# Optimization experiments

Hardware: AMD Instinct MI355X
Metric: run time of the kernel (lower is better)

## Reference

```python
import jax, jax.numpy as jnp
import numpy as np

B, T, C, H = 8, 2048, 1024, 64


def build_rope_cache(seq_len, dim):
    half = dim // 2
    inv_freq = 1.0 / (10000.0 ** (jnp.arange(half, dtype=jnp.float32) / half))
    t = jnp.arange(seq_len, dtype=jnp.float32)
    freqs = t[:, None] * inv_freq[None, :]          # (T, half)
    cos = jnp.repeat(jnp.cos(freqs), 2, axis=-1)    # (T, dim) interleaved
    sin = jnp.repeat(jnp.sin(freqs), 2, axis=-1)
    return cos, sin


def apply_rope(x, cos, sin):
    # x: (B, T, H); cos/sin: (T, H)
    x1 = x[..., ::2]
    x2 = x[..., 1::2]
    rot = jnp.stack([-x2, x1], axis=-1).reshape(x.shape)
    return x * cos[None] + rot * sin[None]


def setup_inputs() -> dict:
    key = jax.random.key(0)
    kx, kq, kk, kv = jax.random.split(key, 4)
    scale = 1.0 / np.sqrt(C)
    return {
        "x": jax.random.normal(kx, (B, T, C), dtype=jnp.float32),
        "Wq": jax.random.normal(kq, (C, H), dtype=jnp.float32) * scale,
        "Wk": jax.random.normal(kk, (C, H), dtype=jnp.float32) * scale,
        "Wv": jax.random.normal(kv, (C, H), dtype=jnp.float32) * scale,
    }


def reference(x, Wq, Wk, Wv):
    Bc, Tc, _ = x.shape
    head_size = Wq.shape[1]
    cos, sin = build_rope_cache(Tc, head_size)

    q = apply_rope(x @ Wq, cos, sin)   # (B, T, H)
    k = apply_rope(x @ Wk, cos, sin)   # (B, T, H)
    v = x @ Wv                          # (B, T, H)

    # full TxT masked softmax attention (matches original non-fused path)
    wei = jnp.einsum('bth,bsh->bts', q, k) * (head_size ** -0.5)  # (B, T, T)
    causal = jnp.tril(jnp.ones((Tc, Tc), dtype=bool))
    wei = jnp.where(causal[None], wei, -jnp.inf)
    wei = jax.nn.softmax(wei, axis=-1)
    # dropout p=0 (eval mode) -> identity
    return jnp.einsum('bts,bsh->bth', wei, v)
```

## Files before the change

### kernel.cpp

```cpp
#include <hip/hip_runtime.h>
#include <cmath>

#define Tn  2048
#define Cn  1024
#define Hn  64
#define BTn 16384

typedef _Float16 f16x8 __attribute__((ext_vector_type(8)));
typedef _Float16 f16x4 __attribute__((ext_vector_type(4)));
typedef _Float16 f16x2 __attribute__((ext_vector_type(2)));
typedef float    f32x4 __attribute__((ext_vector_type(4)));

__global__ __launch_bounds__(256) void prep_w_kernel(
    const float* __restrict__ Wq, const float* __restrict__ Wk,
    const float* __restrict__ Wv, _Float16* __restrict__ Wt)
{
    __shared__ float ts[64][65];
    const int blk = blockIdx.x;
    const int p   = blk >> 4;
    const int c0  = (blk & 15) * 64;
    const float* __restrict__ W = (p == 0) ? Wq : (p == 1) ? Wk : Wv;
    const int tid = threadIdx.x;
    #pragma unroll
    for (int it = 0; it < 16; it++) {
        int idx = tid + it * 256;
        int c = idx >> 6, n = idx & 63;
        ts[c][n] = W[(size_t)(c0 + c) * Hn + n];
    }
    __syncthreads();
    #pragma unroll
    for (int it = 0; it < 16; it++) {
        int idx = tid + it * 256;
        int n = idx >> 6, c = idx & 63;
        Wt[(size_t)(p * 64 + n) * Cn + c0 + c] = (_Float16)ts[c][n];
    }
}

#define XSP 1032

__global__ __launch_bounds__(256) void proj_kernel(
    const float* __restrict__ x, const _Float16* __restrict__ Wt,
    _Float16* __restrict__ qh, _Float16* __restrict__ kh, _Float16* __restrict__ vT)
{
    __shared__ _Float16 xs[32 * XSP];
    const int row0 = blockIdx.x * 32;
    const int tid  = threadIdx.x;
    const int wave = tid >> 6, lane = tid & 63;
    const int quad = lane >> 4, l15 = lane & 15;

    #pragma unroll 8
    for (int it = 0; it < 32; it++) {
        int idx = tid + it * 256;
        int r = idx >> 8, c4 = idx & 255;
        float4 xv = *(const float4*)&x[(size_t)(row0 + r) * Cn + c4 * 4];
        f16x4 hv = { (_Float16)xv.x, (_Float16)xv.y, (_Float16)xv.z, (_Float16)xv.w };
        *(f16x4*)&xs[r * XSP + c4 * 4] = hv;
    }
    __syncthreads();

    f32x4 acc[2][3] = {};
    const _Float16* __restrict__ wb = Wt + (size_t)(wave * 48 + l15) * Cn + quad * 8;

    #pragma unroll 4
    for (int kc = 0; kc < Cn; kc += 32) {
        f16x8 b0 = *(const f16x8*)&wb[kc];
        f16x8 b1 = *(const f16x8*)&wb[16 * Cn + kc];
        f16x8 b2 = *(const f16x8*)&wb[32 * Cn + kc];
        f16x8 a0 = *(const f16x8*)&xs[(     l15) * XSP + kc + quad * 8];
        f16x8 a1 = *(const f16x8*)&xs[(16 + l15) * XSP + kc + quad * 8];
        acc[0][0] = __builtin_amdgcn_mfma_f32_16x16x32_f16(a0, b0, acc[0][0], 0, 0, 0);
        acc[1][0] = __builtin_amdgcn_mfma_f32_16x16x32_f16(a1, b0, acc[1][0], 0, 0, 0);
        acc[0][1] = __builtin_amdgcn_mfma_f32_16x16x32_f16(a0, b1, acc[0][1], 0, 0, 0);
        acc[1][1] = __builtin_amdgcn_mfma_f32_16x16x32_f16(a1, b1, acc[1][1], 0, 0, 0);
        acc[0][2] = __builtin_amdgcn_mfma_f32_16x16x32_f16(a0, b2, acc[0][2], 0, 0, 0);
        acc[1][2] = __builtin_amdgcn_mfma_f32_16x16x32_f16(a1, b2, acc[1][2], 0, 0, 0);
    }

    const int bidx = row0 >> 11;
    #pragma unroll
    for (int nt = 0; nt < 3; nt++) {
        const int n = wave * 48 + nt * 16 + l15;
        const int p = n >> 6;
        const int h = n & 63;
        if (p < 2) {
            _Float16* __restrict__ outb = (p == 0) ? qh : kh;
            const float invf = __expf(-0.2878231366242557f * (float)(h >> 1));
            #pragma unroll
            for (int mt = 0; mt < 2; mt++) {
                #pragma unroll
                for (int r = 0; r < 4; r++) {
                    int   row = row0 + mt * 16 + quad * 4 + r;
                    float val = acc[mt][nt][r];
                    float partner = __shfl_xor(val, 1, 64);
                    float ang = (float)(row & (Tn - 1)) * invf;
                    float sv, cv;
                    __sincosf(ang, &sv, &cv);
                    float res = (h & 1) ? fmaf(val, cv,  partner * sv)
                                        : fmaf(val, cv, -partner * sv);
                    if (p == 0) res *= 0.125f;
                    float resn = __shfl_xor(res, 1, 64);
                    if (!(l15 & 1)) {
                        f16x2 pk = { (_Float16)res, (_Float16)resn };
                        *(f16x2*)&outb[(size_t)row * Hn + h] = pk;
                    }
                }
            }
        } else {
            #pragma unroll
            for (int mt = 0; mt < 2; mt++) {
                int t = (row0 & (Tn - 1)) + mt * 16 + quad * 4;
                f16x4 pv = { (_Float16)acc[mt][nt][0], (_Float16)acc[mt][nt][1],
                             (_Float16)acc[mt][nt][2], (_Float16)acc[mt][nt][3] };
                *(f16x4*)&vT[((size_t)bidx * Hn + h) * Tn + t] = pv;
            }
        }
    }
}

#define PSP 72

__global__ __launch_bounds__(128) void attn_kernel(
    const _Float16* __restrict__ qh, const _Float16* __restrict__ kh,
    const _Float16* __restrict__ vT, float* __restrict__ out)
{
    __shared__ _Float16 ps[2][16 * PSP];
    __shared__ float ocomb[2][16][65];
    __shared__ float mlcomb[2][2][16];

    const int blk = blockIdx.x;
    const int b   = blk & 7;
    const int j   = blk >> 3;
    const int jm  = j & 31, g = j >> 5;
    const int qt  = (g == 0) ? (127 - jm)
                  : (g == 1) ? (64 + jm)
                  : (g == 2) ? (63 - jm) : jm;
    const int t0  = qt * 16;
    const int tid = threadIdx.x;
    const int w = tid >> 6, lane = tid & 63;
    const int quad = lane >> 4, l15 = lane & 15;

    const _Float16* __restrict__ qb = qh + (size_t)b * Tn * Hn;
    const _Float16* __restrict__ kb = kh + (size_t)b * Tn * Hn;
    const _Float16* __restrict__ vb = vT + (size_t)b * Hn * Tn;

    const f16x8 aq0 = *(const f16x8*)&qb[(size_t)(t0 + l15) * Hn +      quad * 8];
    const f16x8 aq1 = *(const f16x8*)&qb[(size_t)(t0 + l15) * Hn + 32 + quad * 8];

    float m_run[4], l_run[4];
    f32x4 oacc[4] = {};
    #pragma unroll
    for (int r = 0; r < 4; r++) { m_run[r] = -1e30f; l_run[r] = 0.0f; }

    const int nst = (t0 + 16 + 63) >> 6;
    for (int jt = w; jt < nst; jt += 2) {
        const int s0 = jt * 64;

        f16x8 kf[4][2];
        #pragma unroll
        for (int nt = 0; nt < 4; nt++) {
            const _Float16* kp = &kb[(size_t)(s0 + nt * 16 + l15) * Hn + quad * 8];
            kf[nt][0] = *(const f16x8*)kp;
            kf[nt][1] = *(const f16x8*)(kp + 32);
        }
        f32x4 sacc[4];
        #pragma unroll
        for (int nt = 0; nt < 4; nt++) {
            f32x4 z = {};
            z = __builtin_amdgcn_mfma_f32_16x16x32_f16(aq0, kf[nt][0], z, 0, 0, 0);
            z = __builtin_amdgcn_mfma_f32_16x16x32_f16(aq1, kf[nt][1], z, 0, 0, 0);
            sacc[nt] = z;
        }

        f16x8 vf[2][4];
        #pragma unroll
        for (int sc = 0; sc < 2; sc++)
            #pragma unroll
            for (int ht = 0; ht < 4; ht++)
                vf[sc][ht] = *(const f16x8*)&vb[(size_t)(ht * 16 + l15) * Tn
                                                + s0 + sc * 32 + quad * 8];

        if (jt == nst - 1) {
            #pragma unroll
            for (int nt = 0; nt < 4; nt++)
                #pragma unroll
                for (int r = 0; r < 4; r++) {
                    int scol = s0 + nt * 16 + l15;
                    int trow = t0 + quad * 4 + r;
                    if (scol > trow) sacc[nt][r] = -1e30f;
                }
        }

        float pr[4][4];
        #pragma unroll
        for (int r = 0; r < 4; r++) {
            float mx = fmaxf(fmaxf(sacc[0][r], sacc[1][r]),
                             fmaxf(sacc[2][r], sacc[3][r]));
            #pragma unroll
            for (int off = 1; off < 16; off <<= 1)
                mx = fmaxf(mx, __shfl_xor(mx, off, 64));
            float mnew  = fmaxf(m_run[r], mx);
            float alpha = __expf(m_run[r] - mnew);
            m_run[r] = mnew;
            float rs = 0.0f;
            #pragma unroll
            for (int nt = 0; nt < 4; nt++) {
                float pv = __expf(sacc[nt][r] - mnew);
                pr[nt][r] = pv; rs += pv;
            }
            #pragma unroll
            for (int off = 1; off < 16; off <<= 1)
                rs += __shfl_xor(rs, off, 64);
            l_run[r] = fmaf(l_run[r], alpha, rs);
            #pragma unroll
            for (int ht = 0; ht < 4; ht++)
                oacc[ht][r] = oacc[ht][r] * alpha;
        }

        #pragma unroll
        for (int nt = 0; nt < 4; nt++)
            #pragma unroll
            for (int r = 0; r < 4; r++) {
                float pv = pr[nt][r];
                float pn = __shfl_xor(pv, 1, 64);
                if (!(l15 & 1)) {
                    f16x2 pk = { (_Float16)pv, (_Float16)pn };
                    *(f16x2*)&ps[w][(quad * 4 + r) * PSP + nt * 16 + l15] = pk;
                }
            }

        #pragma unroll
        for (int sc = 0; sc < 2; sc++) {
            f16x8 ap = *(const f16x8*)&ps[w][l15 * PSP + sc * 32 + quad * 8];
            #pragma unroll
            for (int ht = 0; ht < 4; ht++)
                oacc[ht] = __builtin_amdgcn_mfma_f32_16x16x32_f16(ap, vf[sc][ht],
                                                                  oacc[ht], 0, 0, 0);
        }
    }

    #pragma unroll
    for (int r = 0; r < 4; r++) {
        #pragma unroll
        for (int ht = 0; ht < 4; ht++)
            ocomb[w][quad * 4 + r][ht * 16 + l15] = oacc[ht][r];
        if (l15 == 0) {
            mlcomb[w][0][quad * 4 + r] = m_run[r];
            mlcomb[w][1][quad * 4 + r] = l_run[r];
        }
    }
    __syncthreads();

    #pragma unroll
    for (int rp = 0; rp < 8; rp++) {
        int row = rp * 2 + (lane >> 5);
        int h   = w * 32 + (lane & 31);
        float m0 = mlcomb[0][0][row], m1 = mlcomb[1][0][row];
        float mm = fmaxf(m0, m1);
        float a0 = __expf(m0 - mm), a1 = __expf(m1 - mm);
        float ll = mlcomb[0][1][row] * a0 + mlcomb[1][1][row] * a1;
        float ov = (ocomb[0][row][h] * a0 + ocomb[1][row][h] * a1) / ll;
        out[((size_t)b * Tn + t0 + row) * Hn + h] = ov;
    }
}

extern "C" void kernel_launch(void* const* d_in, const int* in_sizes, int n_in,
                              void* d_out, int out_size, void* d_ws, size_t ws_size,
                              hipStream_t stream) {
    const float* x  = (const float*)d_in[0];
    const float* Wq = (const float*)d_in[1];
    const float* Wk = (const float*)d_in[2];
    const float* Wv = (const float*)d_in[3];

    const size_t qkvN = (size_t)BTn * Hn;
    _Float16* qh = (_Float16*)d_ws;
    _Float16* kh = qh + qkvN;
    _Float16* vT = kh + qkvN;
    _Float16* Wt = vT + qkvN;

    prep_w_kernel<<<48, 256, 0, stream>>>(Wq, Wk, Wv, Wt);
    proj_kernel<<<BTn / 32, 256, 0, stream>>>(x, Wt, qh, kh, vT);
    attn_kernel<<<1024, 128, 0, stream>>>(qh, kh, vT, (float*)d_out);
}
```

Before: 163.5 us.

## Split projection K-loop into two LDS phases and use four waves in attention

The projection kernel now stages x in two halves of 512 columns, which halves its LDS footprint and adds an occupancy hint of four blocks per CU. The attention kernel goes from two to four waves per block, each wave taking every fourth key tile, and the final merge combines four partial softmax states. The aim is more resident waves and more parallel work per query tile, at the cost of an extra barrier in the projection kernel and more LDS and combine work in attention.

```diff
diff --git a/kernel.cpp b/kernel.cpp
--- a/kernel.cpp
+++ b/kernel.cpp
@@ -36,44 +36,49 @@
     }
 }
 
-#define XSP 1032
-
-__global__ __launch_bounds__(256) void proj_kernel(
+#define XS2 520
+
+__global__ __launch_bounds__(256, 4) void proj_kernel(
     const float* __restrict__ x, const _Float16* __restrict__ Wt,
     _Float16* __restrict__ qh, _Float16* __restrict__ kh, _Float16* __restrict__ vT)
 {
-    __shared__ _Float16 xs[32 * XSP];
+    __shared__ _Float16 xs[32 * XS2];
     const int row0 = blockIdx.x * 32;
     const int tid  = threadIdx.x;
     const int wave = tid >> 6, lane = tid & 63;
     const int quad = lane >> 4, l15 = lane & 15;
 
-    #pragma unroll 8
-    for (int it = 0; it < 32; it++) {
-        int idx = tid + it * 256;
-        int r = idx >> 8, c4 = idx & 255;
-        float4 xv = *(const float4*)&x[(size_t)(row0 + r) * Cn + c4 * 4];
-        f16x4 hv = { (_Float16)xv.x, (_Float16)xv.y, (_Float16)xv.z, (_Float16)xv.w };
-        *(f16x4*)&xs[r * XSP + c4 * 4] = hv;
-    }
-    __syncthreads();
-
     f32x4 acc[2][3] = {};
     const _Float16* __restrict__ wb = Wt + (size_t)(wave * 48 + l15) * Cn + quad * 8;
 
-    #pragma unroll 4
-    for (int kc = 0; kc < Cn; kc += 32) {
-        f16x8 b0 = *(const f16x8*)&wb[kc];
-        f16x8 b1 = *(const f16x8*)&wb[16 * Cn + kc];
-        f16x8 b2 = *(const f16x8*)&wb[32 * Cn + kc];
-        f16x8 a0 = *(const f16x8*)&xs[(     l15) * XSP + kc + quad * 8];
-        f16x8 a1 = *(const f16x8*)&xs[(16 + l15) * XSP + kc + quad * 8];
-        acc[0][0] = __builtin_amdgcn_mfma_f32_16x16x32_f16(a0, b0, acc[0][0], 0, 0, 0);
-        acc[1][0] = __builtin_amdgcn_mfma_f32_16x16x32_f16(a1, b0, acc[1][0], 0, 0, 0);
-        acc[0][1] = __builtin_amdgcn_mfma_f32_16x16x32_f16(a0, b1, acc[0][1], 0, 0, 0);
-        acc[1][1] = __builtin_amdgcn_mfma_f32_16x16x32_f16(a1, b1, acc[1][1], 0, 0, 0);
-        acc[0][2] = __builtin_amdgcn_mfma_f32_16x16x32_f16(a0, b2, acc[0][2], 0, 0, 0);
-        acc[1][2] = __builtin_amdgcn_mfma_f32_16x16x32_f16(a1, b2, acc[1][2], 0, 0, 0);
+    #pragma unroll
+    for (int ph = 0; ph < 2; ph++) {
+        if (ph) __syncthreads();
+        #pragma unroll 8
+        for (int it = 0; it < 16; it++) {
+            int idx = tid + it * 256;
+            int r = idx >> 7, c4 = idx & 127;
+            float4 xv = *(const float4*)&x[(size_t)(row0 + r) * Cn + ph * 512 + c4 * 4];
+            f16x4 hv = { (_Float16)xv.x, (_Float16)xv.y, (_Float16)xv.z, (_Float16)xv.w };
+            *(f16x4*)&xs[r * XS2 + c4 * 4] = hv;
+        }
+        __syncthreads();
+
+        const _Float16* __restrict__ wp = wb + ph * 512;
+        #pragma unroll 4
+        for (int kc = 0; kc < 512; kc += 32) {
+            f16x8 b0 = *(const f16x8*)&wp[kc];
+            f16x8 b1 = *(const f16x8*)&wp[16 * Cn + kc];
+            f16x8 b2 = *(const f16x8*)&wp[32 * Cn + kc];
+            f16x8 a0 = *(const f16x8*)&xs[(     l15) * XS2 + kc + quad * 8];
+            f16x8 a1 = *(const f16x8*)&xs[(16 + l15) * XS2 + kc + quad * 8];
+            acc[0][0] = __builtin_amdgcn_mfma_f32_16x16x32_f16(a0, b0, acc[0][0], 0, 0, 0);
+            acc[1][0] = __builtin_amdgcn_mfma_f32_16x16x32_f16(a1, b0, acc[1][0], 0, 0, 0);
+            acc[0][1] = __builtin_amdgcn_mfma_f32_16x16x32_f16(a0, b1, acc[0][1], 0, 0, 0);
+            acc[1][1] = __builtin_amdgcn_mfma_f32_16x16x32_f16(a1, b1, acc[1][1], 0, 0, 0);
+            acc[0][2] = __builtin_amdgcn_mfma_f32_16x16x32_f16(a0, b2, acc[0][2], 0, 0, 0);
+            acc[1][2] = __builtin_amdgcn_mfma_f32_16x16x32_f16(a1, b2, acc[1][2], 0, 0, 0);
+        }
     }
 
     const int bidx = row0 >> 11;
@@ -119,13 +124,13 @@
 
 #define PSP 72
 
-__global__ __launch_bounds__(128) void attn_kernel(
+__global__ __launch_bounds__(256, 4) void attn_kernel(
     const _Float16* __restrict__ qh, const _Float16* __restrict__ kh,
     const _Float16* __restrict__ vT, float* __restrict__ out)
 {
-    __shared__ _Float16 ps[2][16 * PSP];
-    __shared__ float ocomb[2][16][65];
-    __shared__ float mlcomb[2][2][16];
+    __shared__ _Float16 ps[4][16 * PSP];
+    __shared__ float ocomb[4][16][65];
+    __shared__ float mlcomb[4][2][16];
 
     const int blk = blockIdx.x;
     const int b   = blk & 7;
@@ -152,7 +157,7 @@
     for (int r = 0; r < 4; r++) { m_run[r] = -1e30f; l_run[r] = 0.0f; }
 
     const int nst = (t0 + 16 + 63) >> 6;
-    for (int jt = w; jt < nst; jt += 2) {
+    for (int jt = w; jt < nst; jt += 4) {
         const int s0 = jt * 64;
 
         f16x8 kf[4][2];
@@ -251,15 +256,18 @@
     __syncthreads();
 
     #pragma unroll
-    for (int rp = 0; rp < 8; rp++) {
-        int row = rp * 2 + (lane >> 5);
-        int h   = w * 32 + (lane & 31);
+    for (int rp = 0; rp < 4; rp++) {
+        int row = w * 4 + rp;
         float m0 = mlcomb[0][0][row], m1 = mlcomb[1][0][row];
-        float mm = fmaxf(m0, m1);
+        float m2 = mlcomb[2][0][row], m3 = mlcomb[3][0][row];
+        float mm = fmaxf(fmaxf(m0, m1), fmaxf(m2, m3));
         float a0 = __expf(m0 - mm), a1 = __expf(m1 - mm);
-        float ll = mlcomb[0][1][row] * a0 + mlcomb[1][1][row] * a1;
-        float ov = (ocomb[0][row][h] * a0 + ocomb[1][row][h] * a1) / ll;
-        out[((size_t)b * Tn + t0 + row) * Hn + h] = ov;
+        float a2 = __expf(m2 - mm), a3 = __expf(m3 - mm);
+        float ll = mlcomb[0][1][row] * a0 + mlcomb[1][1][row] * a1
+                 + mlcomb[2][1][row] * a2 + mlcomb[3][1][row] * a3;
+        float ov = (ocomb[0][row][lane] * a0 + ocomb[1][row][lane] * a1
+                  + ocomb[2][row][lane] * a2 + ocomb[3][row][lane] * a3) / ll;
+        out[((size_t)b * Tn + t0 + row) * Hn + lane] = ov;
     }
 }
 
@@ -279,5 +287,5 @@
 
     prep_w_kernel<<<48, 256, 0, stream>>>(Wq, Wk, Wv, Wt);
     proj_kernel<<<BTn / 32, 256, 0, stream>>>(x, Wt, qh, kh, vT);
-    attn_kernel<<<1024, 128, 0, stream>>>(qh, kh, vT, (float*)d_out);
-}
+    attn_kernel<<<1024, 256, 0, stream>>>(qh, kh, vT, (float*)d_out);
+}
```

Measured after the change: 157.8 us. 1.04x faster.
